# Kernel tuning notes

Measured on AMD Instinct MI355X. Metric: run time of the kernel, lower is better.

## Reference

```python
import jax, jax.numpy as jnp
import numpy as np

D_MODEL = 1024
NUM_HEADS = 16
HEAD_DIM = D_MODEL // NUM_HEADS  # 64


def setup_inputs() -> dict:
    key = jax.random.key(0)
    ks = jax.random.split(key, 9)
    s = 1.0 / np.sqrt(D_MODEL)
    return {
        "x": jax.random.normal(ks[0], (2, 2048, D_MODEL), dtype=jnp.float32),
        "Wq": jax.random.normal(ks[1], (D_MODEL, D_MODEL), dtype=jnp.float32) * s,
        "bq": jnp.zeros((D_MODEL,), dtype=jnp.float32),
        "Wk": jax.random.normal(ks[2], (D_MODEL, HEAD_DIM), dtype=jnp.float32) * s,
        "bk": jnp.zeros((HEAD_DIM,), dtype=jnp.float32),
        "Wv": jax.random.normal(ks[3], (D_MODEL, HEAD_DIM), dtype=jnp.float32) * s,
        "bv": jnp.zeros((HEAD_DIM,), dtype=jnp.float32),
        "Wo": jax.random.normal(ks[4], (D_MODEL, D_MODEL), dtype=jnp.float32) * s,
        "bo": jnp.zeros((D_MODEL,), dtype=jnp.float32),
    }


def reference(x, Wq, bq, Wk, bk, Wv, bv, Wo, bo):
    B, S, D = x.shape
    H, hd = NUM_HEADS, HEAD_DIM
    # Projections: Q has H heads, K/V a single shared head (MQA).
    Q = (x @ Wq + bq).reshape(B, S, H, hd).transpose(0, 2, 1, 3)  # [B,H,S,hd]
    K = x @ Wk + bk  # [B,S,hd]
    V = x @ Wv + bv  # [B,S,hd]
    # Shared-K/V attention: broadcast K across heads instead of expand().
    scores = jnp.einsum("bhqd,bkd->bhqk", Q, K) / np.sqrt(hd)  # [B,H,S,S]
    attn = jax.nn.softmax(scores, axis=-1)
    attended = jnp.einsum("bhqk,bkd->bhqd", attn, V)  # [B,H,S,hd]
    attended = attended.transpose(0, 2, 1, 3).reshape(B, S, D)
    return attended @ Wo + bo
```

## Files before the change

kernel.cpp:

```cpp
#include <hip/hip_runtime.h>
#include <hip/hip_bf16.h>

#define D_MODEL 1024
#define NHEADS  16
#define HD      64
#define BATCH   2
#define SEQ     2048
#define MROWS   4096
#define NQKV    1152
#define NSPLIT  4

typedef short  short8  __attribute__((ext_vector_type(8)));
typedef float  floatx4 __attribute__((ext_vector_type(4)));

__device__ inline short f2bf(float f) {
  unsigned u = __builtin_bit_cast(unsigned, f);
  u = (u + 0x7FFF + ((u >> 16) & 1)) >> 16;
  return (short)u;
}

__device__ inline unsigned pack_trunc(float lo, float hi) {
  return __builtin_amdgcn_perm(__builtin_bit_cast(unsigned, hi),
                               __builtin_bit_cast(unsigned, lo), 0x07060302u);
}

__device__ inline void async_copy16(const short* g, short* l) {
  __builtin_amdgcn_global_load_lds(
      (const __attribute__((address_space(1))) unsigned int*)g,
      (__attribute__((address_space(3))) unsigned int*)l, 16, 0, 0);
}

__global__ __launch_bounds__(256)
void prep_kernel(const float* __restrict__ x,  const float* __restrict__ Wq,
                 const float* __restrict__ Wk, const float* __restrict__ Wv,
                 const float* __restrict__ Wo, const float* __restrict__ bq,
                 const float* __restrict__ bk, const float* __restrict__ bv,
                 short* __restrict__ xb, short* __restrict__ Wqkv_t,
                 short* __restrict__ Wo_t, float* __restrict__ bqkv) {
  const int id = blockIdx.x;
  const int t  = threadIdx.x;
  if (id < 544) {
    __shared__ short Ts[64 * 72];
    const float* src; short* dst; int N, off, tile;
    if (id < 256)      { src = Wq; dst = Wqkv_t; N = 1024; off = 0;    tile = id; }
    else if (id < 272) { src = Wk; dst = Wqkv_t; N = 64;   off = 1024; tile = id - 256; }
    else if (id < 288) { src = Wv; dst = Wqkv_t; N = 64;   off = 1088; tile = id - 272; }
    else               { src = Wo; dst = Wo_t;   N = 1024; off = 0;    tile = id - 288; }
    const int k0 = (N == 1024) ? (tile & 15) * 64 : tile * 64;
    const int n0 = (N == 1024) ? (tile >> 4) * 64 : 0;
    {
      const int r = t >> 2, c = (t & 3) * 16;
      const float* s = src + (size_t)(k0 + r) * N + n0 + c;
#pragma unroll
      for (int j = 0; j < 16; j += 4) {
        float4 v = *reinterpret_cast<const float4*>(s + j);
        Ts[r * 72 + c + j + 0] = f2bf(v.x); Ts[r * 72 + c + j + 1] = f2bf(v.y);
        Ts[r * 72 + c + j + 2] = f2bf(v.z); Ts[r * 72 + c + j + 3] = f2bf(v.w);
      }
    }
    __syncthreads();
    {
      const int n = t >> 2, kc = (t & 3) * 16;
      short8 o0, o1;
#pragma unroll
      for (int j = 0; j < 8; ++j) o0[j] = Ts[(kc + j) * 72 + n];
#pragma unroll
      for (int j = 0; j < 8; ++j) o1[j] = Ts[(kc + 8 + j) * 72 + n];
      short* d = dst + (size_t)(off + n0 + n) * 1024 + k0 + kc;
      *reinterpret_cast<short8*>(d)     = o0;
      *reinterpret_cast<short8*>(d + 8) = o1;
    }
  } else if (id < 549) {
    const int i = (id - 544) * 256 + t;
    if (i < 1024)      bqkv[i] = bq[i];
    else if (i < 1088) bqkv[i] = bk[i - 1024];
    else if (i < 1152) bqkv[i] = bv[i - 1088];
  } else {
    const int i = ((id - 549) * 256 + t) * 8;
    if (i < MROWS * D_MODEL) {
      float4 a = *reinterpret_cast<const float4*>(x + i);
      float4 b = *reinterpret_cast<const float4*>(x + i + 4);
      short8 o;
      o[0] = f2bf(a.x); o[1] = f2bf(a.y); o[2] = f2bf(a.z); o[3] = f2bf(a.w);
      o[4] = f2bf(b.x); o[5] = f2bf(b.y); o[6] = f2bf(b.z); o[7] = f2bf(b.w);
      *reinterpret_cast<short8*>(xb + i) = o;
    }
  }
}

__global__ __launch_bounds__(256)
void vt_kernel(const short* __restrict__ QKV, short* __restrict__ Vtg) {
  __shared__ short Ts[64 * 72];
  const int b = blockIdx.y, k0 = blockIdx.x * 64;
  const int t = threadIdx.x;
  {
    const int r = t >> 2, c = (t & 3) * 16;
    const short* s = &QKV[(size_t)(b * SEQ + k0 + r) * NQKV + 1088 + c];
    *reinterpret_cast<short8*>(&Ts[r * 72 + c])     = *reinterpret_cast<const short8*>(s);
    *reinterpret_cast<short8*>(&Ts[r * 72 + c + 8]) = *reinterpret_cast<const short8*>(s + 8);
  }
  __syncthreads();
  {
    const int d = t >> 2, kc = (t & 3) * 16;
    short8 o0, o1;
#pragma unroll
    for (int j = 0; j < 8; ++j) o0[j] = Ts[(kc + j) * 72 + d];
#pragma unroll
    for (int j = 0; j < 8; ++j) o1[j] = Ts[(kc + 8 + j) * 72 + d];
    short* dst = &Vtg[(size_t)(b * 64 + d) * SEQ + k0 + kc];
    *reinterpret_cast<short8*>(dst)     = o0;
    *reinterpret_cast<short8*>(dst + 8) = o1;
  }
}

template<bool OUT_BF16, int SCALE_N>
__global__ __launch_bounds__(256)
void gemm_mfma_bt(const short* __restrict__ A, const short* __restrict__ Bt,
                  const float* __restrict__ bias, void* __restrict__ Cout,
                  int M, int N, int K) {
  __shared__ short As[128 * 64];
  __shared__ short Bs[64 * 64];
  const int t    = threadIdx.x;
  const int w    = t >> 6;
  const int lane = t & 63;
  const int quad = lane >> 4;
  const int l16  = lane & 15;
  const int bm   = blockIdx.x * 128;
  const int bn   = blockIdx.y * 64;
  const int wm   = (w >> 1) * 64;
  const int wn   = (w & 1) * 32;

  const int srow = t >> 3;
  const int cc   = ((t & 7) ^ (srow & 7)) * 8;
  const short* gA = A  + (size_t)(bm + srow) * K + cc;
  const short* gB = Bt + (size_t)(bn + srow) * K + cc;
  short* lA = As + t * 8;
  short* lB = Bs + t * 8;

  floatx4 acc[4][2];
#pragma unroll
  for (int i = 0; i < 4; ++i)
#pragma unroll
    for (int j = 0; j < 2; ++j) acc[i][j] = (floatx4){0.f, 0.f, 0.f, 0.f};

  const int xr = l16 & 7;

  for (int k0 = 0; k0 < K; k0 += 64) {
    __syncthreads();
    async_copy16(gA + k0, lA);
    async_copy16(gA + (size_t)32 * K + k0, lA + 2048);
    async_copy16(gA + (size_t)64 * K + k0, lA + 4096);
    async_copy16(gA + (size_t)96 * K + k0, lA + 6144);
    async_copy16(gB + k0, lB);
    async_copy16(gB + (size_t)32 * K + k0, lB + 2048);
    __syncthreads();

    short8 fa0[4], fa1[4], fb0[2], fb1[2];
#pragma unroll
    for (int mi = 0; mi < 4; ++mi) {
      const int row = wm + mi * 16 + l16;
      fa0[mi] = *reinterpret_cast<const short8*>(&As[row * 64 + (quad ^ xr) * 8]);
      fa1[mi] = *reinterpret_cast<const short8*>(&As[row * 64 + ((4 + quad) ^ xr) * 8]);
    }
#pragma unroll
    for (int ni = 0; ni < 2; ++ni) {
      const int row = wn + ni * 16 + l16;
      fb0[ni] = *reinterpret_cast<const short8*>(&Bs[row * 64 + (quad ^ xr) * 8]);
      fb1[ni] = *reinterpret_cast<const short8*>(&Bs[row * 64 + ((4 + quad) ^ xr) * 8]);
    }
#pragma unroll
    for (int mi = 0; mi < 4; ++mi)
#pragma unroll
      for (int ni = 0; ni < 2; ++ni) {
        acc[mi][ni] = __builtin_amdgcn_mfma_f32_16x16x32_bf16(fa0[mi], fb0[ni], acc[mi][ni], 0, 0, 0);
        acc[mi][ni] = __builtin_amdgcn_mfma_f32_16x16x32_bf16(fa1[mi], fb1[ni], acc[mi][ni], 0, 0, 0);
      }
  }

#pragma unroll
  for (int ni = 0; ni < 2; ++ni) {
    const int col = bn + wn + ni * 16 + l16;
    const float bs = bias[col];
    const float sc = (col < SCALE_N) ? 0.18033688f : 1.0f;
#pragma unroll
    for (int mi = 0; mi < 4; ++mi) {
      const int row = bm + wm + mi * 16 + quad * 4;
#pragma unroll
      for (int r = 0; r < 4; ++r) {
        const float v = (acc[mi][ni][r] + bs) * sc;
        if (OUT_BF16)
          ((short*)Cout)[(size_t)(row + r) * N + col] = f2bf(v);
        else
          ((float*)Cout)[(size_t)(row + r) * N + col] = v;
      }
    }
  }
}

__global__ __launch_bounds__(256, 4)
void mqa_flash_bf16(const short* __restrict__ QKV, const short* __restrict__ Vtg,
                    _Float16* __restrict__ Opart, float* __restrict__ lpart) {
  const int bh    = blockIdx.y;
  const int b     = bh >> 4;
  const int h     = bh & 15;
  const int s0    = blockIdx.x * 128;
  const int split = blockIdx.z;
  const int t     = threadIdx.x;
  const int w     = t >> 6;
  const int lane  = t & 63;
  const int quad  = lane >> 4;
  const int l16   = lane & 15;

  __shared__ short KVs[8192];
  __shared__ short Ps[4 * 16 * 72];
  short* Ks   = KVs;
  short* Vt   = KVs + 4096;
  short* myPs = Ps + w * 16 * 72;

  short8 aq[2][2];
#pragma unroll
  for (int st = 0; st < 2; ++st) {
    const short* qrow = &QKV[(size_t)(b * SEQ + s0 + w * 32 + st * 16 + l16) * NQKV + h * HD];
    aq[st][0] = *reinterpret_cast<const short8*>(qrow + quad * 8);
    aq[st][1] = *reinterpret_cast<const short8*>(qrow + 32 + quad * 8);
  }

  floatx4 oacc[2][4];
  floatx4 lacc[2];
#pragma unroll
  for (int st = 0; st < 2; ++st) {
    lacc[st] = (floatx4){0.f, 0.f, 0.f, 0.f};
#pragma unroll
    for (int dg = 0; dg < 4; ++dg) oacc[st][dg] = (floatx4){0.f, 0.f, 0.f, 0.f};
  }

  short8 ones;
#pragma unroll
  for (int j = 0; j < 8; ++j) ones[j] = (short)0x3F80;

  const int srow = t >> 3;
  const int cc   = ((t & 7) ^ (srow & 7)) * 8;
  const short* gK0 = QKV + (size_t)(b * SEQ + srow) * NQKV + 1024 + cc;
  const short* gK1 = gK0 + (size_t)32 * NQKV;
  const short* gV0 = Vtg + (size_t)(b * 64 + srow) * SEQ + cc;
  const short* gV1 = gV0 + (size_t)32 * SEQ;
  short* lK0 = Ks + w * 512;
  short* lK1 = Ks + 2048 + w * 512;
  short* lV0 = Vt + w * 512;
  short* lV1 = Vt + 2048 + w * 512;

  const int xr = l16 & 7;
  const int kbase = split * (SEQ / NSPLIT);

  for (int kk = kbase; kk < kbase + SEQ / NSPLIT; kk += 64) {
    __syncthreads();
    async_copy16(gK0 + (size_t)kk * NQKV, lK0);
    async_copy16(gK1 + (size_t)kk * NQKV, lK1);
    async_copy16(gV0 + kk, lV0);
    async_copy16(gV1 + kk, lV1);
    __syncthreads();

    short8 kb[4][2], vb[4][2];
#pragma unroll
    for (int kg = 0; kg < 4; ++kg) {
      kb[kg][0] = *reinterpret_cast<const short8*>(&Ks[(kg * 16 + l16) * 64 + (quad ^ xr) * 8]);
      kb[kg][1] = *reinterpret_cast<const short8*>(&Ks[(kg * 16 + l16) * 64 + ((4 + quad) ^ xr) * 8]);
    }
#pragma unroll
    for (int dg = 0; dg < 4; ++dg) {
      vb[dg][0] = *reinterpret_cast<const short8*>(&Vt[(dg * 16 + l16) * 64 + (quad ^ xr) * 8]);
      vb[dg][1] = *reinterpret_cast<const short8*>(&Vt[(dg * 16 + l16) * 64 + ((4 + quad) ^ xr) * 8]);
    }

#pragma unroll
    for (int st = 0; st < 2; ++st) {
#pragma unroll
      for (int kg = 0; kg < 4; ++kg) {
        floatx4 s4 = (floatx4){0.f, 0.f, 0.f, 0.f};
        s4 = __builtin_amdgcn_mfma_f32_16x16x32_bf16(kb[kg][0], aq[st][0], s4, 0, 0, 0);
        s4 = __builtin_amdgcn_mfma_f32_16x16x32_bf16(kb[kg][1], aq[st][1], s4, 0, 0, 0);
        float p0 = __builtin_exp2f(s4[0]);
        float p1 = __builtin_exp2f(s4[1]);
        float p2 = __builtin_exp2f(s4[2]);
        float p3 = __builtin_exp2f(s4[3]);
        uint2 pk;
        pk.x = pack_trunc(p0, p1);
        pk.y = pack_trunc(p2, p3);
        *reinterpret_cast<uint2*>(&myPs[l16 * 72 + kg * 16 + quad * 4]) = pk;
      }
      short8 ap0 = *reinterpret_cast<const short8*>(&myPs[l16 * 72 + quad * 8]);
      short8 ap1 = *reinterpret_cast<const short8*>(&myPs[l16 * 72 + 32 + quad * 8]);
      lacc[st] = __builtin_amdgcn_mfma_f32_16x16x32_bf16(ap0, ones, lacc[st], 0, 0, 0);
      lacc[st] = __builtin_amdgcn_mfma_f32_16x16x32_bf16(ap1, ones, lacc[st], 0, 0, 0);
#pragma unroll
      for (int dg = 0; dg < 4; ++dg) {
        oacc[st][dg] = __builtin_amdgcn_mfma_f32_16x16x32_bf16(ap0, vb[dg][0], oacc[st][dg], 0, 0, 0);
        oacc[st][dg] = __builtin_amdgcn_mfma_f32_16x16x32_bf16(ap1, vb[dg][1], oacc[st][dg], 0, 0, 0);
      }
    }
  }

#pragma unroll
  for (int st = 0; st < 2; ++st) {
#pragma unroll
    for (int rg = 0; rg < 4; ++rg) {
      const int qg = s0 + w * 32 + st * 16 + quad * 4 + rg;
      _Float16* dst = Opart + ((size_t)(split * 32 + bh) * SEQ + qg) * 64 + l16;
#pragma unroll
      for (int dg = 0; dg < 4; ++dg) dst[dg * 16] = (_Float16)oacc[st][dg][rg];
      if (l16 == 0) lpart[(size_t)(split * 32 + bh) * SEQ + qg] = lacc[st][rg];
    }
  }
}

__global__ __launch_bounds__(256)
void combine_kernel(const _Float16* __restrict__ Opart, const float* __restrict__ lpart,
                    short* __restrict__ Att) {
  const int idx = blockIdx.x * 256 + threadIdx.x;
  const int r   = idx >> 3;
  const int d0  = (idx & 7) * 8;
  float l = 0.f;
  float o[8] = {0.f,0.f,0.f,0.f,0.f,0.f,0.f,0.f};
#pragma unroll
  for (int s = 0; s < NSPLIT; ++s) {
    const _Float16* op = Opart + ((size_t)(s * 32 * SEQ) + r) * 64 + d0;
    l += lpart[(size_t)s * 32 * SEQ + r];
#pragma unroll
    for (int j = 0; j < 8; ++j) o[j] += (float)op[j];
  }
  const float inv = 1.0f / l;
  short8 ov;
#pragma unroll
  for (int j = 0; j < 8; ++j) ov[j] = f2bf(o[j] * inv);
  const int bhh = r >> 11, q = r & 2047;
  const int bb = bhh >> 4, hh = bhh & 15;
  *reinterpret_cast<short8*>(&Att[(size_t)(bb * SEQ + q) * D_MODEL + hh * HD + d0]) = ov;
}

extern "C" void kernel_launch(void* const* d_in, const int* in_sizes, int n_in,
                              void* d_out, int out_size, void* d_ws, size_t ws_size,
                              hipStream_t stream) {
  const float* x  = (const float*)d_in[0];
  const float* Wq = (const float*)d_in[1];
  const float* bq = (const float*)d_in[2];
  const float* Wk = (const float*)d_in[3];
  const float* bk = (const float*)d_in[4];
  const float* Wv = (const float*)d_in[5];
  const float* bv = (const float*)d_in[6];
  const float* Wo = (const float*)d_in[7];
  const float* bo = (const float*)d_in[8];
  float* out = (float*)d_out;

  short* Wqkv_t = (short*)d_ws;
  short* Wo_t   = Wqkv_t + (size_t)NQKV * D_MODEL;
  short* xb     = Wo_t + (size_t)D_MODEL * D_MODEL;
  short* QKV    = xb + (size_t)MROWS * D_MODEL;
  short* Att    = QKV + (size_t)MROWS * NQKV;
  short* Vtg    = Att + (size_t)MROWS * D_MODEL;
  float* bqkv   = (float*)(Vtg + (size_t)BATCH * HD * SEQ);
  float* lpart  = bqkv + 1152;
  _Float16* Opart = (_Float16*)(lpart + (size_t)NSPLIT * 32 * SEQ);

  prep_kernel<<<2597, 256, 0, stream>>>(x, Wq, Wk, Wv, Wo, bq, bk, bv,
                                        xb, Wqkv_t, Wo_t, bqkv);

  gemm_mfma_bt<true, 1024><<<dim3(MROWS / 128, NQKV / 64), 256, 0, stream>>>(
      xb, Wqkv_t, bqkv, QKV, MROWS, NQKV, D_MODEL);

  vt_kernel<<<dim3(SEQ / 64, BATCH), 256, 0, stream>>>(QKV, Vtg);

  mqa_flash_bf16<<<dim3(SEQ / 128, BATCH * NHEADS, NSPLIT), 256, 0, stream>>>(
      QKV, Vtg, Opart, lpart);

  combine_kernel<<<2048, 256, 0, stream>>>(Opart, lpart, Att);

  gemm_mfma_bt<false, 0><<<dim3(MROWS / 128, D_MODEL / 64), 256, 0, stream>>>(
      Att, Wo_t, bo, out, MROWS, D_MODEL, D_MODEL);
}
```

Baseline: 185.5 us.

## Fuse V transpose into QKV GEMM epilogue, double KV tile, halve key splits

Removes the separate vt_kernel by writing the transposed V directly from the QKV GEMM epilogue as 4-element vector stores. The flash attention kernel now loads 128 keys per barrier pair, using twice the LDS, and its occupancy hint drops from 4 to 3 blocks. NSPLIT goes from 4 to 2, which halves the partial outputs the combine kernel reads but also halves the attention grid's parallelism. The aim is fewer launches, fewer barriers and less partial-result traffic.

```diff
diff --git a/kernel.cpp b/kernel.cpp
--- a/kernel.cpp
+++ b/kernel.cpp
@@ -8,8 +8,9 @@
 #define SEQ     2048
 #define MROWS   4096
 #define NQKV    1152
-#define NSPLIT  4
-
+#define NSPLIT  2
+
+typedef short  short4v __attribute__((ext_vector_type(4)));
 typedef short  short8  __attribute__((ext_vector_type(8)));
 typedef float  floatx4 __attribute__((ext_vector_type(4)));
 
@@ -88,36 +89,11 @@
   }
 }
 
-__global__ __launch_bounds__(256)
-void vt_kernel(const short* __restrict__ QKV, short* __restrict__ Vtg) {
-  __shared__ short Ts[64 * 72];
-  const int b = blockIdx.y, k0 = blockIdx.x * 64;
-  const int t = threadIdx.x;
-  {
-    const int r = t >> 2, c = (t & 3) * 16;
-    const short* s = &QKV[(size_t)(b * SEQ + k0 + r) * NQKV + 1088 + c];
-    *reinterpret_cast<short8*>(&Ts[r * 72 + c])     = *reinterpret_cast<const short8*>(s);
-    *reinterpret_cast<short8*>(&Ts[r * 72 + c + 8]) = *reinterpret_cast<const short8*>(s + 8);
-  }
-  __syncthreads();
-  {
-    const int d = t >> 2, kc = (t & 3) * 16;
-    short8 o0, o1;
-#pragma unroll
-    for (int j = 0; j < 8; ++j) o0[j] = Ts[(kc + j) * 72 + d];
-#pragma unroll
-    for (int j = 0; j < 8; ++j) o1[j] = Ts[(kc + 8 + j) * 72 + d];
-    short* dst = &Vtg[(size_t)(b * 64 + d) * SEQ + k0 + kc];
-    *reinterpret_cast<short8*>(dst)     = o0;
-    *reinterpret_cast<short8*>(dst + 8) = o1;
-  }
-}
-
-template<bool OUT_BF16, int SCALE_N>
+template<bool OUT_BF16, int SCALE_N, bool VT_FUSE>
 __global__ __launch_bounds__(256)
 void gemm_mfma_bt(const short* __restrict__ A, const short* __restrict__ Bt,
                   const float* __restrict__ bias, void* __restrict__ Cout,
-                  int M, int N, int K) {
+                  short* __restrict__ Vtg, int M, int N, int K) {
   __shared__ short As[128 * 64];
   __shared__ short Bs[64 * 64];
   const int t    = threadIdx.x;
@@ -185,19 +161,28 @@
 #pragma unroll
     for (int mi = 0; mi < 4; ++mi) {
       const int row = bm + wm + mi * 16 + quad * 4;
+      short4v vt4;
 #pragma unroll
       for (int r = 0; r < 4; ++r) {
         const float v = (acc[mi][ni][r] + bs) * sc;
-        if (OUT_BF16)
-          ((short*)Cout)[(size_t)(row + r) * N + col] = f2bf(v);
-        else
+        if (OUT_BF16) {
+          const short bv16 = f2bf(v);
+          ((short*)Cout)[(size_t)(row + r) * N + col] = bv16;
+          if (VT_FUSE) vt4[r] = bv16;
+        } else {
           ((float*)Cout)[(size_t)(row + r) * N + col] = v;
-      }
-    }
-  }
-}
-
-__global__ __launch_bounds__(256, 4)
+        }
+      }
+      if (VT_FUSE && col >= 1088) {
+        const int d = col - 1088;
+        const int b = row >> 11, s = row & 2047;
+        *reinterpret_cast<short4v*>(&Vtg[(size_t)(b * 64 + d) * SEQ + s]) = vt4;
+      }
+    }
+  }
+}
+
+__global__ __launch_bounds__(256, 3)
 void mqa_flash_bf16(const short* __restrict__ QKV, const short* __restrict__ Vtg,
                     _Float16* __restrict__ Opart, float* __restrict__ lpart) {
   const int bh    = blockIdx.y;
@@ -211,10 +196,8 @@
   const int quad  = lane >> 4;
   const int l16   = lane & 15;
 
-  __shared__ short KVs[8192];
+  __shared__ short KVs[16384];
   __shared__ short Ps[4 * 16 * 72];
-  short* Ks   = KVs;
-  short* Vt   = KVs + 4096;
   short* myPs = Ps + w * 16 * 72;
 
   short8 aq[2][2];
@@ -244,58 +227,68 @@
   const short* gK1 = gK0 + (size_t)32 * NQKV;
   const short* gV0 = Vtg + (size_t)(b * 64 + srow) * SEQ + cc;
   const short* gV1 = gV0 + (size_t)32 * SEQ;
-  short* lK0 = Ks + w * 512;
-  short* lK1 = Ks + 2048 + w * 512;
-  short* lV0 = Vt + w * 512;
-  short* lV1 = Vt + 2048 + w * 512;
+  short* lK0 = KVs + w * 512;
+  short* lK1 = KVs + 2048 + w * 512;
+  short* lV0 = KVs + 8192 + w * 512;
+  short* lV1 = KVs + 10240 + w * 512;
 
   const int xr = l16 & 7;
   const int kbase = split * (SEQ / NSPLIT);
 
-  for (int kk = kbase; kk < kbase + SEQ / NSPLIT; kk += 64) {
+  for (int kk = kbase; kk < kbase + SEQ / NSPLIT; kk += 128) {
     __syncthreads();
     async_copy16(gK0 + (size_t)kk * NQKV, lK0);
     async_copy16(gK1 + (size_t)kk * NQKV, lK1);
+    async_copy16(gK0 + (size_t)(kk + 64) * NQKV, lK0 + 4096);
+    async_copy16(gK1 + (size_t)(kk + 64) * NQKV, lK1 + 4096);
     async_copy16(gV0 + kk, lV0);
     async_copy16(gV1 + kk, lV1);
-    __syncthreads();
-
-    short8 kb[4][2], vb[4][2];
-#pragma unroll
-    for (int kg = 0; kg < 4; ++kg) {
-      kb[kg][0] = *reinterpret_cast<const short8*>(&Ks[(kg * 16 + l16) * 64 + (quad ^ xr) * 8]);
-      kb[kg][1] = *reinterpret_cast<const short8*>(&Ks[(kg * 16 + l16) * 64 + ((4 + quad) ^ xr) * 8]);
-    }
-#pragma unroll
-    for (int dg = 0; dg < 4; ++dg) {
-      vb[dg][0] = *reinterpret_cast<const short8*>(&Vt[(dg * 16 + l16) * 64 + (quad ^ xr) * 8]);
-      vb[dg][1] = *reinterpret_cast<const short8*>(&Vt[(dg * 16 + l16) * 64 + ((4 + quad) ^ xr) * 8]);
-    }
-
-#pragma unroll
-    for (int st = 0; st < 2; ++st) {
+    async_copy16(gV0 + kk + 64, lV0 + 4096);
+    async_copy16(gV1 + kk + 64, lV1 + 4096);
+    __syncthreads();
+
+#pragma unroll
+    for (int half = 0; half < 2; ++half) {
+      const short* Ks = KVs + half * 4096;
+      const short* Vt = KVs + 8192 + half * 4096;
+
+      short8 kb[4][2], vb[4][2];
 #pragma unroll
       for (int kg = 0; kg < 4; ++kg) {
-        floatx4 s4 = (floatx4){0.f, 0.f, 0.f, 0.f};
-        s4 = __builtin_amdgcn_mfma_f32_16x16x32_bf16(kb[kg][0], aq[st][0], s4, 0, 0, 0);
-        s4 = __builtin_amdgcn_mfma_f32_16x16x32_bf16(kb[kg][1], aq[st][1], s4, 0, 0, 0);
-        float p0 = __builtin_exp2f(s4[0]);
-        float p1 = __builtin_exp2f(s4[1]);
-        float p2 = __builtin_exp2f(s4[2]);
-        float p3 = __builtin_exp2f(s4[3]);
-        uint2 pk;
-        pk.x = pack_trunc(p0, p1);
-        pk.y = pack_trunc(p2, p3);
-        *reinterpret_cast<uint2*>(&myPs[l16 * 72 + kg * 16 + quad * 4]) = pk;
-      }
-      short8 ap0 = *reinterpret_cast<const short8*>(&myPs[l16 * 72 + quad * 8]);
-      short8 ap1 = *reinterpret_cast<const short8*>(&myPs[l16 * 72 + 32 + quad * 8]);
-      lacc[st] = __builtin_amdgcn_mfma_f32_16x16x32_bf16(ap0, ones, lacc[st], 0, 0, 0);
-      lacc[st] = __builtin_amdgcn_mfma_f32_16x16x32_bf16(ap1, ones, lacc[st], 0, 0, 0);
+        kb[kg][0] = *reinterpret_cast<const short8*>(&Ks[(kg * 16 + l16) * 64 + (quad ^ xr) * 8]);
+        kb[kg][1] = *reinterpret_cast<const short8*>(&Ks[(kg * 16 + l16) * 64 + ((4 + quad) ^ xr) * 8]);
+      }
 #pragma unroll
       for (int dg = 0; dg < 4; ++dg) {
-        oacc[st][dg] = __builtin_amdgcn_mfma_f32_16x16x32_bf16(ap0, vb[dg][0], oacc[st][dg], 0, 0, 0);
-        oacc[st][dg] = __builtin_amdgcn_mfma_f32_16x16x32_bf16(ap1, vb[dg][1], oacc[st][dg], 0, 0, 0);
+        vb[dg][0] = *reinterpret_cast<const short8*>(&Vt[(dg * 16 + l16) * 64 + (quad ^ xr) * 8]);
+        vb[dg][1] = *reinterpret_cast<const short8*>(&Vt[(dg * 16 + l16) * 64 + ((4 + quad) ^ xr) * 8]);
+      }
+
+#pragma unroll
+      for (int st = 0; st < 2; ++st) {
+#pragma unroll
+        for (int kg = 0; kg < 4; ++kg) {
+          floatx4 s4 = (floatx4){0.f, 0.f, 0.f, 0.f};
+          s4 = __builtin_amdgcn_mfma_f32_16x16x32_bf16(kb[kg][0], aq[st][0], s4, 0, 0, 0);
+          s4 = __builtin_amdgcn_mfma_f32_16x16x32_bf16(kb[kg][1], aq[st][1], s4, 0, 0, 0);
+          float p0 = __builtin_exp2f(s4[0]);
+          float p1 = __builtin_exp2f(s4[1]);
+          float p2 = __builtin_exp2f(s4[2]);
+          float p3 = __builtin_exp2f(s4[3]);
+          uint2 pk;
+          pk.x = pack_trunc(p0, p1);
+          pk.y = pack_trunc(p2, p3);
+          *reinterpret_cast<uint2*>(&myPs[l16 * 72 + kg * 16 + quad * 4]) = pk;
+        }
+        short8 ap0 = *reinterpret_cast<const short8*>(&myPs[l16 * 72 + quad * 8]);
+        short8 ap1 = *reinterpret_cast<const short8*>(&myPs[l16 * 72 + 32 + quad * 8]);
+        lacc[st] = __builtin_amdgcn_mfma_f32_16x16x32_bf16(ap0, ones, lacc[st], 0, 0, 0);
+        lacc[st] = __builtin_amdgcn_mfma_f32_16x16x32_bf16(ap1, ones, lacc[st], 0, 0, 0);
+#pragma unroll
+        for (int dg = 0; dg < 4; ++dg) {
+          oacc[st][dg] = __builtin_amdgcn_mfma_f32_16x16x32_bf16(ap0, vb[dg][0], oacc[st][dg], 0, 0, 0);
+          oacc[st][dg] = __builtin_amdgcn_mfma_f32_16x16x32_bf16(ap1, vb[dg][1], oacc[st][dg], 0, 0, 0);
+        }
       }
     }
   }
@@ -364,16 +357,14 @@
   prep_kernel<<<2597, 256, 0, stream>>>(x, Wq, Wk, Wv, Wo, bq, bk, bv,
                                         xb, Wqkv_t, Wo_t, bqkv);
 
-  gemm_mfma_bt<true, 1024><<<dim3(MROWS / 128, NQKV / 64), 256, 0, stream>>>(
-      xb, Wqkv_t, bqkv, QKV, MROWS, NQKV, D_MODEL);
-
-  vt_kernel<<<dim3(SEQ / 64, BATCH), 256, 0, stream>>>(QKV, Vtg);
+  gemm_mfma_bt<true, 1024, true><<<dim3(MROWS / 128, NQKV / 64), 256, 0, stream>>>(
+      xb, Wqkv_t, bqkv, QKV, Vtg, MROWS, NQKV, D_MODEL);
 
   mqa_flash_bf16<<<dim3(SEQ / 128, BATCH * NHEADS, NSPLIT), 256, 0, stream>>>(
       QKV, Vtg, Opart, lpart);
 
   combine_kernel<<<2048, 256, 0, stream>>>(Opart, lpart, Att);
 
-  gemm_mfma_bt<false, 0><<<dim3(MROWS / 128, D_MODEL / 64), 256, 0, stream>>>(
-      Att, Wo_t, bo, out, MROWS, D_MODEL, D_MODEL);
-}
+  gemm_mfma_bt<false, 0, false><<<dim3(MROWS / 128, D_MODEL / 64), 256, 0, stream>>>(
+      Att, Wo_t, bo, out, nullptr, MROWS, D_MODEL, D_MODEL);
+}
```

Measured after the change: 181.1 us. -2.3%, faster.
